# Kernel tuning notes

Hardware: AMD Instinct MI355X
Metric: run time of the kernel (lower is better)

Reference implementation:

```python
import jax, jax.numpy as jnp
import numpy as np

N_EMBD = 1024
N_HEAD = 16
HEAD_SIZE = N_EMBD // N_HEAD  # 64
B, T = 4, 2048

def setup_inputs() -> dict:
    key = jax.random.key(0)
    k1, k2, k3, k4 = jax.random.split(key, 4)
    x = jax.random.normal(k1, (B, T, N_EMBD), dtype=jnp.float32)
    # weights stored as [in, out]; torch Linear does x @ W.T with W [out,in]
    w_qkv = jax.random.normal(k2, (N_EMBD, 3 * N_EMBD), dtype=jnp.float32) * (N_EMBD ** -0.5)
    w_proj = jax.random.normal(k3, (N_EMBD, N_EMBD), dtype=jnp.float32) * (N_EMBD ** -0.5)
    b_proj = jax.random.normal(k4, (N_EMBD,), dtype=jnp.float32) * 0.01
    return {"x": x, "w_qkv": w_qkv, "w_proj": w_proj, "b_proj": b_proj}

def reference(x, w_qkv, w_proj, b_proj):
    Bx, Tx, C = x.shape
    H, D = N_HEAD, HEAD_SIZE
    qkv = x @ w_qkv                               # [B,T,3C]
    q, k, v = jnp.split(qkv, 3, axis=-1)
    q = q.reshape(Bx, Tx, H, D).transpose(0, 2, 1, 3)  # [B,H,T,D]
    k = k.reshape(Bx, Tx, H, D).transpose(0, 2, 1, 3)
    v = v.reshape(Bx, Tx, H, D).transpose(0, 2, 1, 3)
    att = jnp.einsum('bhqd,bhkd->bhqk', q, k) * (D ** -0.5)  # [B,H,T,T]
    causal = jnp.tril(jnp.ones((Tx, Tx), dtype=bool))
    att = jnp.where(causal[None, None], att, -jnp.inf)
    att = jax.nn.softmax(att, axis=-1)
    out = jnp.einsum('bhqk,bhkd->bhqd', att, v)   # [B,H,T,D]
    out = out.transpose(0, 2, 1, 3).reshape(Bx, Tx, H * D)
    return out @ w_proj + b_proj
```

## Files before the change

kernel.cpp:

```cpp
#include <hip/hip_runtime.h>
#include <hip/hip_bf16.h>
#include <stdint.h>
#include <math.h>


typedef __attribute__((ext_vector_type(8))) short short8;
typedef __attribute__((ext_vector_type(4))) float f32x4;

#define LOG2E 1.44269504088896340736f
#define QSCALE 0.18033688011112042f

__device__ int g_isf32;

__device__ __forceinline__ void gl16(const void* g, void* l) {
  __builtin_amdgcn_global_load_lds(
      (const __attribute__((address_space(1))) unsigned int*)g,
      (__attribute__((address_space(3))) unsigned int*)l, 16, 0, 0);
}

__device__ __forceinline__ short f2bf(float f) {
  __hip_bfloat16 h = __float2bfloat16(f);
  return *reinterpret_cast<short*>(&h);
}
__device__ __forceinline__ float bf2f(short s) {
  __hip_bfloat16 h = *reinterpret_cast<__hip_bfloat16*>(&s);
  return __bfloat162float(h);
}
__device__ __forceinline__ short8 pack8(f32x4 lo, f32x4 hi) {
  short8 r;
#pragma unroll
  for (int e = 0; e < 4; ++e) { r[e] = f2bf(lo[e]); r[4 + e] = f2bf(hi[e]); }
  return r;
}

__device__ __forceinline__ unsigned cvtpk(float a, float b) {
  unsigned r;
  asm("v_cvt_pk_bf16_f32 %0, %1, %2" : "=v"(r) : "v"(a), "v"(b));
  return r;
}

__device__ __forceinline__ float dpp_sum16(float x) {
  int i;
  i = __builtin_amdgcn_update_dpp(0, __builtin_bit_cast(int, x), 0xB1, 0xF, 0xF, true);
  x += __builtin_bit_cast(float, i);
  i = __builtin_amdgcn_update_dpp(0, __builtin_bit_cast(int, x), 0x4E, 0xF, 0xF, true);
  x += __builtin_bit_cast(float, i);
  i = __builtin_amdgcn_update_dpp(0, __builtin_bit_cast(int, x), 0x141, 0xF, 0xF, true);
  x += __builtin_bit_cast(float, i);
  i = __builtin_amdgcn_update_dpp(0, __builtin_bit_cast(int, x), 0x140, 0xF, 0xF, true);
  x += __builtin_bit_cast(float, i);
  return x;
}

__global__ __launch_bounds__(256) void detect_dtype(const unsigned short* w) {
  __shared__ int cnt;
  if (threadIdx.x == 0) cnt = 0;
  __syncthreads();
  const unsigned short* p = w + (long)blockIdx.x * 49152;
  int c = 0;
  for (int i = threadIdx.x; i < 49152; i += 256)
    if (((p[i] >> 7) & 0xFF) == 0xFF) c++;
  atomicAdd(&cnt, c);
  __syncthreads();
  if (threadIdx.x == 0) g_isf32 = (cnt > 8) ? 1 : 0;
}

__global__ __launch_bounds__(256) void cvt_x(const void* __restrict__ src,
                                             short* __restrict__ dst) {
  const long i = ((long)blockIdx.x * 256 + threadIdx.x) * 8;
  if (g_isf32) {
    const float* s = (const float*)src + i;
    *(short8*)(dst + i) = pack8(*(const f32x4*)s, *(const f32x4*)(s + 4));
  } else {
    *(short8*)(dst + i) = *(const short8*)((const short*)src + i);
  }
}

template <int MODE>
__global__ __launch_bounds__(512, 2) void gemm_bt(
    const short* __restrict__ A, const short* __restrict__ Bt,
    const void* __restrict__ bias, void* __restrict__ C,
    short* __restrict__ vt, int M, int N, int K)
{
  __shared__ __align__(16) short As[3][16384];
  __shared__ __align__(16) short Bs[3][8192];
  const int tid  = threadIdx.x;
  const int lane = tid & 63;
  const int wave = tid >> 6;
  const int quad = lane >> 4;
  const int l16  = lane & 15;
  const int wm = (wave >> 1) * 64;
  const int wn = (wave & 1) * 64;

  const int gx = (int)gridDim.x;
  const int nwg = gx * (int)gridDim.y;
  int lb = (int)blockIdx.y * gx + (int)blockIdx.x;
  if ((nwg & 7) == 0) lb = (lb & 7) * (nwg >> 3) + (lb >> 3);
  const long m0 = (long)(lb / gx) * 256;
  const long n0 = (long)(lb % gx) * 128;

  int isf32 = 0;
  if (MODE == 1) {
    isf32 = g_isf32;
    asm volatile("s_waitcnt vmcnt(0) lgkmcnt(0)" ::: "memory");
  }

  f32x4 acc[4][4] = {};

  const int srow = tid >> 3;
  const int scol = ((tid & 7) ^ (srow & 7)) * 8;
  const short* Ag = A  + (m0 + srow) * (long)K + scol;
  const short* Bg = Bt + (n0 + srow) * (long)K + scol;
  const long rs64 = (long)64 * K;

  const int x7  = l16 & 7;
  const int xo0 = ((0 + quad) ^ x7) * 16;
  const int xo1 = ((4 + quad) ^ x7) * 16;
  const int aRow = (wm + l16) * 128;
  const int bRow = (wn + l16) * 128;

  auto STAGE_HALF = [&](int t2, int h) {
    const int bb = t2 % 3;
    const long k0 = (long)t2 << 6;
    gl16(Ag + k0 + (h * 2 + 0) * rs64, (char*)As[bb] + (h * 2 + 0) * 8192 + tid * 16);
    gl16(Ag + k0 + (h * 2 + 1) * rs64, (char*)As[bb] + (h * 2 + 1) * 8192 + tid * 16);
    gl16(Bg + k0 + h * rs64,           (char*)Bs[bb] + h * 8192 + tid * 16);
  };

  const int nt = K >> 6;
  STAGE_HALF(0, 0); STAGE_HALF(0, 1);
  STAGE_HALF(1, 0); STAGE_HALF(1, 1);

  for (int t = 0; t < nt; ++t) {
    if (t + 1 < nt) { asm volatile("s_waitcnt vmcnt(6)" ::: "memory"); }
    else            { asm volatile("s_waitcnt vmcnt(0)" ::: "memory"); }
    __builtin_amdgcn_sched_barrier(0);
    __builtin_amdgcn_s_barrier();
    __builtin_amdgcn_sched_barrier(0);

    const char* Ab = (const char*)As[t % 3];
    const char* Bb = (const char*)Bs[t % 3];

#pragma unroll
    for (int ph = 0; ph < 2; ++ph) {
      const int xo = ph ? xo1 : xo0;
      short8 af[4], bfv[4];
#pragma unroll
      for (int i = 0; i < 4; ++i)
        af[i] = *(const short8*)(Ab + aRow + i * 2048 + xo);
#pragma unroll
      for (int j = 0; j < 4; ++j)
        bfv[j] = *(const short8*)(Bb + bRow + j * 2048 + xo);
      if (t + 2 < nt) STAGE_HALF(t + 2, ph);
      __builtin_amdgcn_s_setprio(1);
#pragma unroll
      for (int i = 0; i < 4; ++i)
#pragma unroll
        for (int j = 0; j < 4; ++j)
          acc[i][j] = __builtin_amdgcn_mfma_f32_16x16x32_bf16(af[i], bfv[j], acc[i][j], 0, 0, 0);
      __builtin_amdgcn_s_setprio(0);
      if (ph == 0) {
        __builtin_amdgcn_s_barrier();
        __builtin_amdgcn_sched_barrier(0);
      }
    }
  }

#pragma unroll
  for (int j = 0; j < 4; ++j) {
    const long col = n0 + wn + j * 16 + l16;
    if (MODE == 2 && col >= 2048) {
      const long hd = col - 2048;
      const long bb = (m0 + wm) >> 11;
      const long tb = (m0 + wm) & 2047;
      short* vrow = vt + ((bb * 16 + (hd >> 6)) * 64 + (hd & 63)) * 2048 + tb;
#pragma unroll
      for (int ip = 0; ip < 2; ++ip)
#pragma unroll
        for (int r = 0; r < 4; ++r)
          *(unsigned*)&vrow[ip * 32 + 2 * (quad * 4 + r)] =
              cvtpk(acc[2 * ip][j][r], acc[2 * ip + 1][j][r]);
    } else {
      float bv = 0.f;
      if (MODE == 1)
        bv = isf32 ? ((const float*)bias)[col] : bf2f(((const short*)bias)[col]);
#pragma unroll
      for (int i = 0; i < 4; ++i) {
        const long row0 = m0 + wm + i * 16 + quad * 4;
#pragma unroll
        for (int r = 0; r < 4; ++r) {
          const long row = row0 + r;
          const float val = acc[i][j][r] + bv;
          if (MODE == 2) {
            const float vq = (col < 1024) ? val * QSCALE : val;
            ((short*)C)[row * 2048 + col] = f2bf(vq);
          } else {
            if (isf32) ((float*)C)[row * (long)N + col] = val;
            else       ((short*)C)[row * (long)N + col] = f2bf(val);
          }
        }
      }
    }
  }
}

__global__ __launch_bounds__(256) void transpose64(
    const void* __restrict__ src, short* __restrict__ dst, int R, int C)
{
  __shared__ __align__(16) short tile[64][72];
  const int isf32 = g_isf32;
  const int tid = threadIdx.x;
  const long r0 = (long)blockIdx.y * 64;
  const long c0 = (long)blockIdx.x * 64;
#pragma unroll
  for (int it = 0; it < 2; ++it) {
    int idx = it * 256 + tid;
    int rr = idx >> 3, ch = idx & 7;
    const long off = (r0 + rr) * C + c0 + ch * 8;
    short8 v;
    if (isf32) {
      const float* s = (const float*)src + off;
      v = pack8(*(const f32x4*)s, *(const f32x4*)(s + 4));
    } else {
      v = *(const short8*)((const short*)src + off);
    }
    *(short8*)&tile[rr][ch * 8] = v;
  }
  __syncthreads();
#pragma unroll
  for (int it = 0; it < 2; ++it) {
    int idx = it * 256 + tid;
    int cc = idx >> 3, ch = idx & 7;
    short8 v;
#pragma unroll
    for (int jj = 0; jj < 8; ++jj) v[jj] = tile[ch * 8 + jj][cc];
    *(short8*)&dst[(c0 + cc) * R + r0 + ch * 8] = v;
  }
}

__global__ __launch_bounds__(512) void attn_fwd(
    const short* __restrict__ qk, const short* __restrict__ vt,
    short* __restrict__ out)
{
  __shared__ __align__(16) short Ks[3][2][64][32];
  __shared__ __align__(16) short Vs[3][2][64][32];
  __shared__ __align__(16) unsigned Pw[8][16][36];
  const int tid = threadIdx.x;
  const int lane = tid & 63, wave = tid >> 6;
  const int quad = lane >> 4, l16 = lane & 15;
  const int bh = blockIdx.x;
  const int b = bh >> 4, h = bh & 15;

  const int shalf = tid >> 8;
  const int srow  = (tid >> 2) & 63;
  const int sc    = (tid & 3) ^ (srow & 3);
  const short* kg = qk + (long)b * 2048 * 2048 + 1024 + h * 64
                      + (long)srow * 2048 + shalf * 32 + sc * 8;
  const short* vg = vt + ((long)bh * 64 + srow) * 2048 + shalf * 32 + sc * 8;

  const int fx = (quad ^ (l16 & 3)) * 16;

  for (int seg = 0; seg < 2; ++seg) {
    const int s = seg ? (15 - (int)blockIdx.y) : (int)blockIdx.y;
    const int nt = 2 * s + 2;
    const int qb = s * 128 + wave * 16;
    const int qlast = qb + 15;

    if (seg) __syncthreads();

    const short* qp = qk + ((long)(b * 2048 + qb + l16)) * 2048 + h * 64 + quad * 8;
    const short8 aq0 = *(const short8*)qp;
    const short8 aq1 = *(const short8*)(qp + 32);

    gl16(kg,                    (char*)Ks[0] + tid * 16);
    gl16(vg,                    (char*)Vs[0] + tid * 16);
    gl16(kg + (long)64 * 2048,  (char*)Ks[1] + tid * 16);
    gl16(vg + 64,               (char*)Vs[1] + tid * 16);

    f32x4 o[4] = {};
    float l_run[4] = {0.f, 0.f, 0.f, 0.f};

    for (int kt = 0; kt < nt; ++kt) {
      if (kt + 1 < nt) { asm volatile("s_waitcnt vmcnt(2)" ::: "memory"); }
      else             { asm volatile("s_waitcnt vmcnt(0)" ::: "memory"); }
      __builtin_amdgcn_sched_barrier(0);
      __builtin_amdgcn_s_barrier();
      __builtin_amdgcn_sched_barrier(0);
      if (kt + 2 < nt) {
        const int rb = (kt + 2) % 3;
        gl16(kg + (long)((kt + 2) * 64) * 2048, (char*)Ks[rb] + tid * 16);
        gl16(vg + (kt + 2) * 64,                (char*)Vs[rb] + tid * 16);
      }

      const int k0 = kt * 64;
      if (k0 > qlast) continue;
      const int rb0 = kt % 3;
      const bool full = (k0 + 63 <= qb);
      const bool h2 = (k0 + 32 <= qlast);

      float p[4][4];
#pragma unroll
      for (int c = 0; c < 4; ++c) {
        if (full || (k0 + c * 16 <= qlast)) {
          short8 kf0 = *(const short8*)((const char*)&Ks[rb0][0][c * 16 + l16][0] + fx);
          short8 kf1 = *(const short8*)((const char*)&Ks[rb0][1][c * 16 + l16][0] + fx);
          f32x4 z = {};
          z = __builtin_amdgcn_mfma_f32_16x16x32_bf16(aq0, kf0, z, 0, 0, 0);
          z = __builtin_amdgcn_mfma_f32_16x16x32_bf16(aq1, kf1, z, 0, 0, 0);
          if (!full) {
#pragma unroll
            for (int r = 0; r < 4; ++r)
              z[r] = (k0 + c * 16 + l16 > qb + quad * 4 + r) ? -1e30f : z[r];
          }
#pragma unroll
          for (int r = 0; r < 4; ++r) {
            p[c][r] = __builtin_amdgcn_exp2f(z[r]);
            l_run[r] += p[c][r];
          }
        } else {
#pragma unroll
          for (int r = 0; r < 4; ++r) p[c][r] = 0.f;
        }
      }
#pragma unroll
      for (int r = 0; r < 4; ++r) {
        Pw[wave][quad * 4 + r][l16] = cvtpk(p[0][r], p[1][r]);
        if (h2) Pw[wave][quad * 4 + r][16 + l16] = cvtpk(p[2][r], p[3][r]);
      }

      {
        short8 pf0 = *(const short8*)&Pw[wave][l16][quad * 4];
#pragma unroll
        for (int i = 0; i < 4; ++i) {
          short8 vf0 = *(const short8*)((const char*)&Vs[rb0][0][i * 16 + l16][0] + fx);
          o[i] = __builtin_amdgcn_mfma_f32_16x16x32_bf16(pf0, vf0, o[i], 0, 0, 0);
        }
        if (h2) {
          short8 pf1 = *(const short8*)&Pw[wave][l16][16 + quad * 4];
#pragma unroll
          for (int i = 0; i < 4; ++i) {
            short8 vf1 = *(const short8*)((const char*)&Vs[rb0][1][i * 16 + l16][0] + fx);
            o[i] = __builtin_amdgcn_mfma_f32_16x16x32_bf16(pf1, vf1, o[i], 0, 0, 0);
          }
        }
      }
    }

#pragma unroll
    for (int r = 0; r < 4; ++r) l_run[r] = dpp_sum16(l_run[r]);
    float inv[4];
#pragma unroll
    for (int r = 0; r < 4; ++r) inv[r] = 1.0f / l_run[r];
    short* op = out + ((long)(b * 2048 + qb + quad * 4)) * 1024 + h * 64;
#pragma unroll
    for (int i = 0; i < 4; ++i)
#pragma unroll
      for (int r = 0; r < 4; ++r)
        op[(long)r * 1024 + i * 16 + l16] = f2bf(o[i][r] * inv[r]);
  }
}

__global__ __launch_bounds__(256) void copy_out(const void* __restrict__ src,
                                                void* __restrict__ dst)
{
  const long n16 = g_isf32 ? 2097152L : 1048576L;
  const uint4* s = (const uint4*)src;
  uint4* d = (uint4*)dst;
  for (long i = (long)blockIdx.x * 256 + threadIdx.x; i < n16;
       i += (long)gridDim.x * 256)
    d[i] = s[i];
}

extern "C" void kernel_launch(void* const* d_in, const int* in_sizes, int n_in,
                              void* d_out, int out_size, void* d_ws, size_t ws_size,
                              hipStream_t stream)
{
  const void* x      = d_in[0];
  const void* w_qkv  = d_in[1];
  const void* w_proj = d_in[2];
  const void* b_proj = d_in[3];

  short* ws = (short*)d_ws;
  const bool planA = ws_size >= 67108864ULL;

  short* qk  = ws;
  short* vtp = ws + 16777216L;

  short *wqkvT, *attnb, *wprojT, *xbf;
  void*  projC;
  if (planA) {
    attnb  = ws + 25165824L;
    wqkvT  = attnb;
    wprojT = qk;
    xbf    = (short*)d_out;
    projC  = d_out;
  } else {
    wqkvT  = (short*)d_out;
    xbf    = (short*)d_out + 3145728L;
    attnb  = (short*)d_out;
    wprojT = vtp;
    projC  = qk;
  }

  detect_dtype<<<64, 256, 0, stream>>>((const unsigned short*)w_qkv);
  cvt_x<<<4096, 256, 0, stream>>>(x, xbf);
  transpose64<<<dim3(3072 / 64, 1024 / 64), 256, 0, stream>>>(w_qkv, wqkvT, 1024, 3072);
  gemm_bt<2><<<dim3(3072 / 128, 8192 / 256), 512, 0, stream>>>(
      xbf, wqkvT, nullptr, qk, vtp, 8192, 3072, 1024);
  attn_fwd<<<dim3(64, 8), 512, 0, stream>>>(qk, vtp, attnb);
  transpose64<<<dim3(1024 / 64, 1024 / 64), 256, 0, stream>>>(w_proj, wprojT, 1024, 1024);
  gemm_bt<1><<<dim3(1024 / 128, 8192 / 256), 512, 0, stream>>>(
      attnb, wprojT, b_proj, projC, nullptr, 8192, 1024, 1024);
  if (!planA)
    copy_out<<<2048, 256, 0, stream>>>(projC, d_out);
}
```

Before: 279.7 us.

## Give each attention wave 32 query rows to reuse K/V fragments

The attention kernel now runs 4 waves of 256 threads instead of 8, and each wave handles two 16-row query sub-tiles. K and V fragments are loaded from LDS once per tile and reused for both sub-tiles, which halves LDS fragment reads per MFMA. Each thread issues four global-to-LDS loads per tile instead of two, and the waitcnt is adjusted to match. The cost is more registers per thread (two accumulators and K/V fragment arrays), fewer waves per block to hide latency, and coarser causal skipping at 32-row granularity.

```diff
diff --git a/kernel.cpp b/kernel.cpp
--- a/kernel.cpp
+++ b/kernel.cpp
@@ -238,125 +238,149 @@
   }
 }
 
-__global__ __launch_bounds__(512) void attn_fwd(
+__global__ __launch_bounds__(256) void attn_fwd(
     const short* __restrict__ qk, const short* __restrict__ vt,
     short* __restrict__ out)
 {
   __shared__ __align__(16) short Ks[3][2][64][32];
   __shared__ __align__(16) short Vs[3][2][64][32];
-  __shared__ __align__(16) unsigned Pw[8][16][36];
+  __shared__ __align__(16) unsigned Pw[4][32][36];
   const int tid = threadIdx.x;
   const int lane = tid & 63, wave = tid >> 6;
   const int quad = lane >> 4, l16 = lane & 15;
   const int bh = blockIdx.x;
   const int b = bh >> 4, h = bh & 15;
 
-  const int shalf = tid >> 8;
-  const int srow  = (tid >> 2) & 63;
-  const int sc    = (tid & 3) ^ (srow & 3);
+  const int sr = tid >> 2;
+  const int sc = (tid & 3) ^ (sr & 3);
   const short* kg = qk + (long)b * 2048 * 2048 + 1024 + h * 64
-                      + (long)srow * 2048 + shalf * 32 + sc * 8;
-  const short* vg = vt + ((long)bh * 64 + srow) * 2048 + shalf * 32 + sc * 8;
+                      + (long)sr * 2048 + sc * 8;
+  const short* vg = vt + ((long)bh * 64 + sr) * 2048 + sc * 8;
 
   const int fx = (quad ^ (l16 & 3)) * 16;
 
   for (int seg = 0; seg < 2; ++seg) {
     const int s = seg ? (15 - (int)blockIdx.y) : (int)blockIdx.y;
     const int nt = 2 * s + 2;
-    const int qb = s * 128 + wave * 16;
-    const int qlast = qb + 15;
+    const int qw = s * 128 + wave * 32;
 
     if (seg) __syncthreads();
 
-    const short* qp = qk + ((long)(b * 2048 + qb + l16)) * 2048 + h * 64 + quad * 8;
-    const short8 aq0 = *(const short8*)qp;
-    const short8 aq1 = *(const short8*)(qp + 32);
-
-    gl16(kg,                    (char*)Ks[0] + tid * 16);
-    gl16(vg,                    (char*)Vs[0] + tid * 16);
-    gl16(kg + (long)64 * 2048,  (char*)Ks[1] + tid * 16);
-    gl16(vg + 64,               (char*)Vs[1] + tid * 16);
-
-    f32x4 o[4] = {};
-    float l_run[4] = {0.f, 0.f, 0.f, 0.f};
+    const short* qp = qk + ((long)(b * 2048 + qw + l16)) * 2048 + h * 64 + quad * 8;
+    short8 aq[2][2];
+    aq[0][0] = *(const short8*)qp;
+    aq[0][1] = *(const short8*)(qp + 32);
+    aq[1][0] = *(const short8*)(qp + 16 * 2048);
+    aq[1][1] = *(const short8*)(qp + 16 * 2048 + 32);
+
+#pragma unroll
+    for (int t = 0; t < 2; ++t) {
+      gl16(kg + (long)(t * 64) * 2048,      (char*)Ks[t][0] + tid * 16);
+      gl16(kg + (long)(t * 64) * 2048 + 32, (char*)Ks[t][1] + tid * 16);
+      gl16(vg + t * 64,                     (char*)Vs[t][0] + tid * 16);
+      gl16(vg + t * 64 + 32,                (char*)Vs[t][1] + tid * 16);
+    }
+
+    f32x4 o[2][4] = {};
+    float l_run[2][4] = {};
 
     for (int kt = 0; kt < nt; ++kt) {
-      if (kt + 1 < nt) { asm volatile("s_waitcnt vmcnt(2)" ::: "memory"); }
+      if (kt + 1 < nt) { asm volatile("s_waitcnt vmcnt(4)" ::: "memory"); }
       else             { asm volatile("s_waitcnt vmcnt(0)" ::: "memory"); }
       __builtin_amdgcn_sched_barrier(0);
       __builtin_amdgcn_s_barrier();
       __builtin_amdgcn_sched_barrier(0);
       if (kt + 2 < nt) {
         const int rb = (kt + 2) % 3;
-        gl16(kg + (long)((kt + 2) * 64) * 2048, (char*)Ks[rb] + tid * 16);
-        gl16(vg + (kt + 2) * 64,                (char*)Vs[rb] + tid * 16);
+        const long k2 = (long)((kt + 2) * 64);
+        gl16(kg + k2 * 2048,      (char*)Ks[rb][0] + tid * 16);
+        gl16(kg + k2 * 2048 + 32, (char*)Ks[rb][1] + tid * 16);
+        gl16(vg + k2,             (char*)Vs[rb][0] + tid * 16);
+        gl16(vg + k2 + 32,        (char*)Vs[rb][1] + tid * 16);
       }
 
       const int k0 = kt * 64;
-      if (k0 > qlast) continue;
+      if (k0 > qw + 31) continue;
       const int rb0 = kt % 3;
-      const bool full = (k0 + 63 <= qb);
-      const bool h2 = (k0 + 32 <= qlast);
-
-      float p[4][4];
-#pragma unroll
-      for (int c = 0; c < 4; ++c) {
-        if (full || (k0 + c * 16 <= qlast)) {
-          short8 kf0 = *(const short8*)((const char*)&Ks[rb0][0][c * 16 + l16][0] + fx);
-          short8 kf1 = *(const short8*)((const char*)&Ks[rb0][1][c * 16 + l16][0] + fx);
-          f32x4 z = {};
-          z = __builtin_amdgcn_mfma_f32_16x16x32_bf16(aq0, kf0, z, 0, 0, 0);
-          z = __builtin_amdgcn_mfma_f32_16x16x32_bf16(aq1, kf1, z, 0, 0, 0);
-          if (!full) {
-#pragma unroll
-            for (int r = 0; r < 4; ++r)
-              z[r] = (k0 + c * 16 + l16 > qb + quad * 4 + r) ? -1e30f : z[r];
+      const bool full = (k0 + 63 <= qw);
+      const bool h2 = (k0 + 32 <= qw + 31);
+
+      short8 kf[4][2];
+#pragma unroll
+      for (int c = 0; c < 4; ++c)
+        if (c < 2 || h2) {
+          kf[c][0] = *(const short8*)((const char*)&Ks[rb0][0][c * 16 + l16][0] + fx);
+          kf[c][1] = *(const short8*)((const char*)&Ks[rb0][1][c * 16 + l16][0] + fx);
+        }
+
+#pragma unroll
+      for (int hh = 0; hh < 2; ++hh) {
+        const int qbh = qw + hh * 16;
+        float p[4][4];
+#pragma unroll
+        for (int c = 0; c < 4; ++c) {
+          if (c < 2 || h2) {
+            f32x4 z = {};
+            z = __builtin_amdgcn_mfma_f32_16x16x32_bf16(aq[hh][0], kf[c][0], z, 0, 0, 0);
+            z = __builtin_amdgcn_mfma_f32_16x16x32_bf16(aq[hh][1], kf[c][1], z, 0, 0, 0);
+            if (!full) {
+#pragma unroll
+              for (int r = 0; r < 4; ++r)
+                z[r] = (k0 + c * 16 + l16 > qbh + quad * 4 + r) ? -1e30f : z[r];
+            }
+#pragma unroll
+            for (int r = 0; r < 4; ++r) {
+              p[c][r] = __builtin_amdgcn_exp2f(z[r]);
+              l_run[hh][r] += p[c][r];
+            }
           }
-#pragma unroll
-          for (int r = 0; r < 4; ++r) {
-            p[c][r] = __builtin_amdgcn_exp2f(z[r]);
-            l_run[r] += p[c][r];
+        }
+#pragma unroll
+        for (int r = 0; r < 4; ++r) {
+          Pw[wave][hh * 16 + quad * 4 + r][l16] = cvtpk(p[0][r], p[1][r]);
+          if (h2)
+            Pw[wave][hh * 16 + quad * 4 + r][16 + l16] = cvtpk(p[2][r], p[3][r]);
+        }
+      }
+
+      {
+        short8 vf[4][2];
+#pragma unroll
+        for (int i = 0; i < 4; ++i) {
+          vf[i][0] = *(const short8*)((const char*)&Vs[rb0][0][i * 16 + l16][0] + fx);
+          if (h2)
+            vf[i][1] = *(const short8*)((const char*)&Vs[rb0][1][i * 16 + l16][0] + fx);
+        }
+#pragma unroll
+        for (int hh = 0; hh < 2; ++hh) {
+          short8 pf0 = *(const short8*)&Pw[wave][hh * 16 + l16][quad * 4];
+#pragma unroll
+          for (int i = 0; i < 4; ++i)
+            o[hh][i] = __builtin_amdgcn_mfma_f32_16x16x32_bf16(pf0, vf[i][0], o[hh][i], 0, 0, 0);
+          if (h2) {
+            short8 pf1 = *(const short8*)&Pw[wave][hh * 16 + l16][16 + quad * 4];
+#pragma unroll
+            for (int i = 0; i < 4; ++i)
+              o[hh][i] = __builtin_amdgcn_mfma_f32_16x16x32_bf16(pf1, vf[i][1], o[hh][i], 0, 0, 0);
           }
-        } else {
-#pragma unroll
-          for (int r = 0; r < 4; ++r) p[c][r] = 0.f;
         }
       }
-#pragma unroll
-      for (int r = 0; r < 4; ++r) {
-        Pw[wave][quad * 4 + r][l16] = cvtpk(p[0][r], p[1][r]);
-        if (h2) Pw[wave][quad * 4 + r][16 + l16] = cvtpk(p[2][r], p[3][r]);
-      }
-
-      {
-        short8 pf0 = *(const short8*)&Pw[wave][l16][quad * 4];
-#pragma unroll
-        for (int i = 0; i < 4; ++i) {
-          short8 vf0 = *(const short8*)((const char*)&Vs[rb0][0][i * 16 + l16][0] + fx);
-          o[i] = __builtin_amdgcn_mfma_f32_16x16x32_bf16(pf0, vf0, o[i], 0, 0, 0);
-        }
-        if (h2) {
-          short8 pf1 = *(const short8*)&Pw[wave][l16][16 + quad * 4];
-#pragma unroll
-          for (int i = 0; i < 4; ++i) {
-            short8 vf1 = *(const short8*)((const char*)&Vs[rb0][1][i * 16 + l16][0] + fx);
-            o[i] = __builtin_amdgcn_mfma_f32_16x16x32_bf16(pf1, vf1, o[i], 0, 0, 0);
-          }
-        }
-      }
-    }
-
-#pragma unroll
-    for (int r = 0; r < 4; ++r) l_run[r] = dpp_sum16(l_run[r]);
-    float inv[4];
-#pragma unroll
-    for (int r = 0; r < 4; ++r) inv[r] = 1.0f / l_run[r];
-    short* op = out + ((long)(b * 2048 + qb + quad * 4)) * 1024 + h * 64;
-#pragma unroll
-    for (int i = 0; i < 4; ++i)
-#pragma unroll
-      for (int r = 0; r < 4; ++r)
-        op[(long)r * 1024 + i * 16 + l16] = f2bf(o[i][r] * inv[r]);
+    }
+
+#pragma unroll
+    for (int hh = 0; hh < 2; ++hh) {
+      float lr[4], inv[4];
+#pragma unroll
+      for (int r = 0; r < 4; ++r) lr[r] = dpp_sum16(l_run[hh][r]);
+#pragma unroll
+      for (int r = 0; r < 4; ++r) inv[r] = 1.0f / lr[r];
+      short* op = out + ((long)(b * 2048 + qw + hh * 16 + quad * 4)) * 1024 + h * 64;
+#pragma unroll
+      for (int i = 0; i < 4; ++i)
+#pragma unroll
+        for (int r = 0; r < 4; ++r)
+          op[(long)r * 1024 + i * 16 + l16] = f2bf(o[hh][i][r] * inv[r]);
+    }
   }
 }
 
@@ -407,7 +431,7 @@
   transpose64<<<dim3(3072 / 64, 1024 / 64), 256, 0, stream>>>(w_qkv, wqkvT, 1024, 3072);
   gemm_bt<2><<<dim3(3072 / 128, 8192 / 256), 512, 0, stream>>>(
       xbf, wqkvT, nullptr, qk, vtp, 8192, 3072, 1024);
-  attn_fwd<<<dim3(64, 8), 512, 0, stream>>>(qk, vtp, attnb);
+  attn_fwd<<<dim3(64, 8), 256, 0, stream>>>(qk, vtp, attnb);
   transpose64<<<dim3(1024 / 64, 1024 / 64), 256, 0, stream>>>(w_proj, wprojT, 1024, 1024);
   gemm_bt<1><<<dim3(1024 / 128, 8192 / 256), 512, 0, stream>>>(
       attnb, wprojT, b_proj, projC, nullptr, 8192, 1024, 1024);
```

New measurement: 288.1 us. 1.03x slower.
